# Kernel tuning notes

Hardware: AMD Instinct MI355X
Metric: run time of the kernel (lower is better)

Reference implementation:

```python
import jax, jax.numpy as jnp
import numpy as np

N, J, H, O, SD = 6144, 2000, 100, 6144, 2


def setup_inputs() -> dict:
    key = jax.random.key(0)
    ks = jax.random.split(key, 18)
    sc = lambda fan_in: 1.0 / np.sqrt(fan_in)
    inp = {
        "gene_expr": jax.random.normal(ks[0], (N, J), jnp.float32),
        "spatial_pos": jax.random.normal(ks[1], (N, SD), jnp.float32),
        # linear weights stored [in, out] (y = x @ W + b)
        "Wq": jax.random.normal(ks[2], (J, H), jnp.float32) * sc(J),
        "bq": jnp.zeros((H,), jnp.float32),
        "Wk": jax.random.normal(ks[3], (J, H), jnp.float32) * sc(J),
        "bk": jnp.zeros((H,), jnp.float32),
        "Wv": jax.random.normal(ks[4], (J, O), jnp.float32) * sc(J),
        "bv": jnp.zeros((O,), jnp.float32),
        "Ws": jax.random.normal(ks[5], (SD, H), jnp.float32) * sc(SD),
        "bs": jnp.zeros((H,), jnp.float32),
        "W1": jax.random.normal(ks[6], (H, H), jnp.float32) * sc(H),
        "b1": jnp.zeros((H,), jnp.float32),
        "W2": jax.random.normal(ks[7], (H, H), jnp.float32) * sc(H),
        "b2": jnp.zeros((H,), jnp.float32),
        "Wf": jax.random.normal(ks[8], (H, 1), jnp.float32) * sc(H),
        "bf": jnp.zeros((1,), jnp.float32),
    }
    return inp


def reference(gene_expr, spatial_pos, Wq, bq, Wk, bk, Wv, bv, Ws, bs,
              W1, b1, W2, b2, Wf, bf):
    dk = jnp.sqrt(jnp.asarray(H, gene_expr.dtype))

    Q = gene_expr @ Wq + bq            # [N,H]
    K = gene_expr @ Wk + bk            # [N,H]
    V = gene_expr @ Wv + bv            # [N,O]

    # advanced spatial scalar + pairwise tanh difference
    sp = spatial_pos @ Ws + bs                             # [N,H]
    enh = jax.nn.relu(jnp.tanh(sp @ W1 + b1) @ W2 + b2)    # [N,H]
    f = (enh @ Wf + bf)[:, 0]                              # [N]
    fdiff = jnp.tanh(f[:, None] - f[None, :])              # [N,N]

    # gaussian kernel of squared pairwise distances (cdist p=2, sigma=1)
    sq = jnp.sum(spatial_pos * spatial_pos, axis=1)
    d2 = jnp.maximum(sq[:, None] + sq[None, :] - 2.0 * (spatial_pos @ spatial_pos.T), 0.0)
    spatial_sim = jnp.exp(-d2 / 2.0)                       # [N,N]

    # row-wise cosine similarity of gene expression
    norm = jnp.linalg.norm(gene_expr, axis=1, keepdims=True)
    xn = gene_expr / jnp.maximum(norm, 1e-12)
    cos_sim = xn @ xn.T                                    # [N,N]

    logits = (Q @ K.T) / dk + spatial_sim + cos_sim + fdiff
    attn = jax.nn.softmax(logits, axis=-1)                 # stable softmax == max-subtract in src
    out = attn @ V                                         # [N,O]
    return attn, out
```

## Files before the change

### kernel.cpp

```cpp
#include <hip/hip_runtime.h>
#include <stdint.h>
#include <math.h>

#define NN 6144
#define JJ 2000
#define HH 100
#define KB 2176
#define XOFF 128
#define KQK 2048

typedef __bf16 bf16;
typedef __bf16 bf16x8 __attribute__((ext_vector_type(8)));
typedef float f32x4 __attribute__((ext_vector_type(4)));

__device__ __forceinline__ void load_lds16(const void* g, void* l) {
  __builtin_amdgcn_global_load_lds(
      (const __attribute__((address_space(1))) void*)(uintptr_t)g,
      (__attribute__((address_space(3))) void*)(uint32_t)(uintptr_t)l,
      16, 0, 0);
}

template <int MODE>
__global__ __launch_bounds__(256, 2) void gemm_bt(
    const bf16* __restrict__ A, const bf16* __restrict__ B,
    int lda, int ldb, int kdim,
    const float* __restrict__ p0, const float* __restrict__ p1,
    const float* __restrict__ p2,
    bf16* __restrict__ ob0, bf16* __restrict__ ob1,
    float* __restrict__ of0, float* __restrict__ rowsum)
{
  __shared__ alignas(16) bf16 As[128 * 64];
  __shared__ alignas(16) bf16 Bs[128 * 64];

  const int tid = threadIdx.x;
  const int lane = tid & 63;
  const int wv = tid >> 6;
  const int m0 = blockIdx.x * 128;
  const int n0 = blockIdx.y * 128;

  const int srow = lane >> 3;
  const int scol = ((lane & 7) ^ srow) * 8;
  const bf16* gA = A + (size_t)(m0 + wv * 32 + srow) * lda + scol;
  const bf16* gB = B + (size_t)(n0 + wv * 32 + srow) * ldb + scol;
  bf16* lA0 = &As[(wv * 32) * 64];
  bf16* lB0 = &Bs[(wv * 32) * 64];

  const int l15 = lane & 15;
  const int l4 = lane >> 4;
  const int s7 = l15 & 7;
  const int wm = (wv >> 1) * 64;
  const int wn = (wv & 1) * 64;
  const bf16* ra0 = &As[(wm + l15) * 64 + ((l4 ^ s7) * 8)];
  const bf16* ra1 = &As[(wm + l15) * 64 + (((l4 + 4) ^ s7) * 8)];
  const bf16* rb0 = &Bs[(wn + l15) * 64 + ((l4 ^ s7) * 8)];
  const bf16* rb1 = &Bs[(wn + l15) * 64 + (((l4 + 4) ^ s7) * 8)];

  f32x4 acc[4][4];
#pragma unroll
  for (int i = 0; i < 4; ++i)
#pragma unroll
    for (int j = 0; j < 4; ++j) acc[i][j] = {0.f, 0.f, 0.f, 0.f};

  const int kiters = kdim >> 6;
  for (int kt = 0; kt < kiters; ++kt) {
    __syncthreads();
#pragma unroll
    for (int it = 0; it < 4; ++it) {
      load_lds16(gA + (size_t)it * 8 * lda, lA0 + it * 512);
      load_lds16(gB + (size_t)it * 8 * ldb, lB0 + it * 512);
    }
    gA += 64;
    gB += 64;
    __syncthreads();
#pragma unroll
    for (int ks = 0; ks < 2; ++ks) {
      const bf16* ra = ks ? ra1 : ra0;
      const bf16* rb = ks ? rb1 : rb0;
      bf16x8 af[4], bb[4];
#pragma unroll
      for (int i = 0; i < 4; ++i)
        af[i] = *(const bf16x8*)(ra + i * 1024);
#pragma unroll
      for (int j = 0; j < 4; ++j)
        bb[j] = *(const bf16x8*)(rb + j * 1024);
#pragma unroll
      for (int i = 0; i < 4; ++i)
#pragma unroll
        for (int j = 0; j < 4; ++j)
          acc[i][j] = __builtin_amdgcn_mfma_f32_16x16x32_bf16(af[i], bb[j], acc[i][j], 0, 0, 0);
    }
  }

  const int row_base = m0 + wm + l4 * 4;
  const int col_base = n0 + wn + l15;

  if (MODE == 0) {
    float sqc[4], fc[4], pxc[4], pyc[4];
#pragma unroll
    for (int j = 0; j < 4; ++j) {
      int c = col_base + j * 16;
      sqc[j] = p0[c];
      fc[j] = p1[c];
      pxc[j] = p2[2 * c];
      pyc[j] = p2[2 * c + 1];
    }
#pragma unroll
    for (int i = 0; i < 4; ++i) {
#pragma unroll
      for (int r = 0; r < 4; ++r) {
        int row = row_base + i * 16 + r;
        float sqr = p0[row], fr = p1[row];
        float pxr = p2[2 * row], pyr = p2[2 * row + 1];
        float rs = 0.f;
#pragma unroll
        for (int j = 0; j < 4; ++j) {
          int c = col_base + j * 16;
          float d2 = fmaxf(sqr + sqc[j] - 2.f * (pxr * pxc[j] + pyr * pyc[j]), 0.f);
          float lg = acc[i][j][r] + __expf(-0.5f * d2) + tanhf(fr - fc[j]);
          float e = __expf(lg);
          ob0[(size_t)row * NN + c] = (bf16)e;
          rs += e;
        }
        rs += __shfl_xor(rs, 1);
        rs += __shfl_xor(rs, 2);
        rs += __shfl_xor(rs, 4);
        rs += __shfl_xor(rs, 8);
        if (l15 == 0) atomicAdd(&rowsum[row], rs);
      }
    }
  } else if (MODE == 1) {
    float nc[4];
#pragma unroll
    for (int j = 0; j < 4; ++j) nc[j] = p0[col_base + j * 16];
#pragma unroll
    for (int i = 0; i < 4; ++i) {
#pragma unroll
      for (int r = 0; r < 4; ++r) {
        int row = row_base + i * 16 + r;
        float bvr = p1[row];
#pragma unroll
        for (int j = 0; j < 4; ++j)
          ob0[(size_t)row * NN + col_base + j * 16] = (bf16)(acc[i][j][r] * nc[j] + bvr);
      }
    }
  } else if (MODE == 2) {
#pragma unroll
    for (int i = 0; i < 4; ++i) {
#pragma unroll
      for (int r = 0; r < 4; ++r) {
        int row = row_base + i * 16 + r;
        float rinv = 1.f / p0[row];
#pragma unroll
        for (int j = 0; j < 4; ++j)
          of0[(size_t)row * NN + col_base + j * 16] = acc[i][j][r] * rinv;
      }
    }
  } else {
#pragma unroll
    for (int i = 0; i < 4; ++i) {
#pragma unroll
      for (int r = 0; r < 4; ++r) {
        int row = row_base + i * 16 + r;
        float nm = p0[row];
#pragma unroll
        for (int j = 0; j < 4; ++j) {
          int h = col_base + j * 16;
          float v = acc[i][j][r] * nm;
          if (h < HH) ob0[(size_t)row * KB + h] = (bf16)((v + p1[h]) * 0.1f);
          else if (h < 2 * HH) ob1[(size_t)row * KB + (h - HH)] = (bf16)(v + p2[h - HH]);
        }
      }
    }
  }
}

__global__ void prep_xn(const float* __restrict__ gene, bf16* __restrict__ Ab,
                        bf16* __restrict__ Bb, float* __restrict__ normv)
{
  int row = blockIdx.x, tid = threadIdx.x;
  const float* g = gene + (size_t)row * JJ;
  float s = 0.f;
  for (int k = tid; k < JJ; k += 256) { float v = g[k]; s += v * v; }
#pragma unroll
  for (int m = 32; m >= 1; m >>= 1) s += __shfl_xor(s, m);
  __shared__ float red[4];
  if ((tid & 63) == 0) red[tid >> 6] = s;
  __syncthreads();
  float tot = red[0] + red[1] + red[2] + red[3];
  float nrm = sqrtf(tot);
  float rinv = 1.f / fmaxf(nrm, 1e-12f);
  if (tid == 0) normv[row] = nrm;
  bf16* a = Ab + (size_t)row * KB;
  bf16* b = Bb + (size_t)row * KB;
  for (int k = tid; k < JJ; k += 256) {
    bf16 v = (bf16)(g[k] * rinv);
    a[XOFF + k] = v;
    b[XOFF + k] = v;
  }
  if (tid < 28) { a[HH + tid] = (bf16)0.f; b[HH + tid] = (bf16)0.f; }
  if (tid < 48) { a[XOFF + JJ + tid] = (bf16)0.f; b[XOFF + JJ + tid] = (bf16)0.f; }
}

__global__ void prep_sf(const float* __restrict__ spos,
                        const float* __restrict__ Ws, const float* __restrict__ bs,
                        const float* __restrict__ W1, const float* __restrict__ b1,
                        const float* __restrict__ W2, const float* __restrict__ b2,
                        const float* __restrict__ Wf, const float* __restrict__ bfp,
                        float* __restrict__ sqv, float* __restrict__ fv)
{
  int row = blockIdx.x, tid = threadIdx.x;
  float px = spos[2 * row], py = spos[2 * row + 1];
  if (tid == 0) sqv[row] = px * px + py * py;
  __shared__ float sp[HH], t1[HH], e2[HH];
  if (tid < HH) sp[tid] = px * Ws[tid] + py * Ws[HH + tid] + bs[tid];
  __syncthreads();
  if (tid < HH) {
    float s = b1[tid];
    for (int gi = 0; gi < HH; ++gi) s += sp[gi] * W1[gi * HH + tid];
    t1[tid] = tanhf(s);
  }
  __syncthreads();
  if (tid < HH) {
    float s = b2[tid];
    for (int gi = 0; gi < HH; ++gi) s += t1[gi] * W2[gi * HH + tid];
    e2[tid] = fmaxf(s, 0.f) * Wf[tid];
  }
  __syncthreads();
  if (tid < 64) {
    float s = e2[tid] + ((tid < 36) ? e2[tid + 64] : 0.f);
#pragma unroll
    for (int m = 32; m >= 1; m >>= 1) s += __shfl_xor(s, m);
    if (tid == 0) fv[row] = s + bfp[0];
  }
}

__global__ void pack_wqk(const float* __restrict__ Wq, const float* __restrict__ Wk,
                         bf16* __restrict__ Wt)
{
  int idx = blockIdx.x * 256 + threadIdx.x;
  int h = idx >> 11;
  int k = idx & 2047;
  float v = 0.f;
  if (k < JJ) {
    if (h < HH) v = Wq[(size_t)k * HH + h];
    else if (h < 2 * HH) v = Wk[(size_t)k * HH + (h - HH)];
  }
  Wt[idx] = (bf16)v;
}

__global__ void pack_wvt(const float* __restrict__ Wv, bf16* __restrict__ Wt)
{
  __shared__ float tile[32][33];
  int tx = threadIdx.x & 31, ty = threadIdx.x >> 5;
  int o0 = blockIdx.x * 32, j0 = blockIdx.y * 32;
#pragma unroll
  for (int rr = 0; rr < 32; rr += 8) {
    int j = j0 + ty + rr;
    tile[ty + rr][tx] = (j < JJ) ? Wv[(size_t)j * NN + o0 + tx] : 0.f;
  }
  __syncthreads();
#pragma unroll
  for (int rr = 0; rr < 32; rr += 8) {
    int o = o0 + ty + rr;
    Wt[(size_t)o * KB + XOFF + j0 + tx] = (bf16)tile[tx][ty + rr];
  }
}

__global__ void zero_wvt_head(bf16* __restrict__ Wt)
{
  int idx = blockIdx.x * 256 + threadIdx.x;
  int o = idx >> 7, c = idx & 127;
  Wt[(size_t)o * KB + c] = (bf16)0.f;
}

__global__ void norm_attn(const bf16* __restrict__ P, const float* __restrict__ rowsum,
                          float* __restrict__ attn)
{
  int row = blockIdx.x;
  float rinv = 1.f / rowsum[row];
  const bf16x8* p = (const bf16x8*)(P + (size_t)row * NN);
  float* dst = attn + (size_t)row * NN;
  for (int c = threadIdx.x; c < NN / 8; c += 256) {
    bf16x8 v = p[c];
#pragma unroll
    for (int e = 0; e < 8; ++e) dst[c * 8 + e] = (float)v[e] * rinv;
  }
}

extern "C" void kernel_launch(void* const* d_in, const int* in_sizes, int n_in,
                              void* d_out, int out_size, void* d_ws, size_t ws_size,
                              hipStream_t stream)
{
  const float* gene = (const float*)d_in[0];
  const float* spos = (const float*)d_in[1];
  const float* Wq = (const float*)d_in[2];
  const float* bq = (const float*)d_in[3];
  const float* Wk = (const float*)d_in[4];
  const float* bk = (const float*)d_in[5];
  const float* Wv = (const float*)d_in[6];
  const float* bv = (const float*)d_in[7];
  const float* Ws = (const float*)d_in[8];
  const float* bs = (const float*)d_in[9];
  const float* W1 = (const float*)d_in[10];
  const float* b1 = (const float*)d_in[11];
  const float* W2 = (const float*)d_in[12];
  const float* b2 = (const float*)d_in[13];
  const float* Wf = (const float*)d_in[14];
  const float* bfp = (const float*)d_in[15];

  char* ws = (char*)d_ws;
  bf16* Abig = (bf16*)ws;            ws += (size_t)NN * KB * 2;
  bf16* Bbig = (bf16*)ws;            ws += (size_t)NN * KB * 2;
  bf16* WvT  = (bf16*)ws;            ws += (size_t)NN * KB * 2;
  bf16* WqkT = (bf16*)ws;            ws += (size_t)256 * KQK * 2;
  bf16* P    = (bf16*)ws;            ws += (size_t)NN * NN * 2;
  float* rowsum = (float*)ws;        ws += (size_t)NN * 4;
  float* normv  = (float*)ws;        ws += (size_t)NN * 4;
  float* sqv    = (float*)ws;        ws += (size_t)NN * 4;
  float* fv     = (float*)ws;        ws += (size_t)NN * 4;

  float* attn = (float*)d_out;
  float* outp = (float*)d_out + (size_t)NN * NN;
  bf16* Vt = (bf16*)d_out;

  hipMemsetAsync(rowsum, 0, NN * sizeof(float), stream);
  prep_xn<<<NN, 256, 0, stream>>>(gene, Abig, Bbig, normv);
  prep_sf<<<NN, 128, 0, stream>>>(spos, Ws, bs, W1, b1, W2, b2, Wf, bfp, sqv, fv);
  pack_wqk<<<(256 * KQK) / 256, 256, 0, stream>>>(Wq, Wk, WqkT);
  pack_wvt<<<dim3(NN / 32, KQK / 32), 256, 0, stream>>>(Wv, WvT);
  zero_wvt_head<<<(NN * XOFF) / 256, 256, 0, stream>>>(WvT);

  gemm_bt<3><<<dim3(NN / 128, 2), 256, 0, stream>>>(
      Abig + XOFF, WqkT, KB, KQK, KQK, normv, bq, bk, Abig, Bbig, nullptr, nullptr);
  gemm_bt<0><<<dim3(NN / 128, NN / 128), 256, 0, stream>>>(
      Abig, Bbig, KB, KB, KB, sqv, fv, spos, P, nullptr, nullptr, rowsum);
  gemm_bt<1><<<dim3(NN / 128, NN / 128), 256, 0, stream>>>(
      WvT, Bbig, KB, KB, KB, normv, bv, nullptr, Vt, nullptr, nullptr, nullptr);
  gemm_bt<2><<<dim3(NN / 128, NN / 128), 256, 0, stream>>>(
      P, Vt, NN, NN, NN, rowsum, nullptr, nullptr, nullptr, nullptr, outp, nullptr);
  norm_attn<<<NN, 256, 0, stream>>>(P, rowsum, attn);
}
```

Baseline: 1.291 ms.

## Replace 128-tile GEMMs with 256x256 pipelined kernel and merge logits/V GEMMs

Adds a 256x256-tile, 512-thread GEMM core with swizzled LDS, double-buffered direct-to-LDS loads, interleaved MFMA phases with setprio, and a block-index swizzle for L2 locality. The logits and V GEMMs, which share the B operand, now run as a single launch split over blockIdx.z, and P@V uses the same core. The aim is more data reuse per tile and fewer launches, traded against much higher register and LDS pressure and more complex barrier and waitcnt choreography.

```diff
diff --git a/kernel.cpp b/kernel.cpp
--- a/kernel.cpp
+++ b/kernel.cpp
@@ -95,22 +95,221 @@
   const int col_base = n0 + wn + l15;
 
   if (MODE == 0) {
+  } else if (MODE == 1) {
+  } else if (MODE == 2) {
+  } else {
+#pragma unroll
+    for (int i = 0; i < 4; ++i) {
+#pragma unroll
+      for (int r = 0; r < 4; ++r) {
+        int row = row_base + i * 16 + r;
+        float nm = p0[row];
+#pragma unroll
+        for (int j = 0; j < 4; ++j) {
+          int h = col_base + j * 16;
+          float v = acc[i][j][r] * nm;
+          if (h < HH) ob0[(size_t)row * KB + h] = (bf16)((v + p1[h]) * 0.1f);
+          else if (h < 2 * HH) ob1[(size_t)row * KB + (h - HH)] = (bf16)(v + p2[h - HH]);
+        }
+      }
+    }
+  }
+}
+
+__device__ __forceinline__ void gemm256_core(
+    const bf16* __restrict__ A, const bf16* __restrict__ B,
+    int lda, int ldb, int kdim, int m0, int n0, f32x4 (&acc)[8][4])
+{
+  __shared__ alignas(16) bf16 As[2][256 * 64];
+  __shared__ alignas(16) bf16 Bs[2][256 * 64];
+
+  const int tid = threadIdx.x;
+  const int lane = tid & 63;
+  const int wv = tid >> 6;
+  const int wm = wv >> 2;
+  const int wn = wv & 3;
+  const int l15 = lane & 15;
+  const int l4 = lane >> 4;
+  const int s7 = lane & 7;
+  const int srow = lane >> 3;
+  const int scol = ((lane & 7) ^ srow) * 8;
+
+  const bf16* gA = A + (size_t)(m0 + wv * 8 + srow) * lda + scol;
+  const bf16* gB = B + (size_t)(n0 + wv * 8 + srow) * ldb + scol;
+
+  const int c0 = (l4 ^ s7) * 8;
+  const int c1 = ((l4 + 4) ^ s7) * 8;
+
+#pragma unroll
+  for (int i = 0; i < 8; ++i)
+#pragma unroll
+    for (int j = 0; j < 4; ++j) acc[i][j] = {0.f, 0.f, 0.f, 0.f};
+
+  const int kt = kdim >> 6;
+
+#define SA_(bufi, h, T)                                                        \
+  do {                                                                         \
+    load_lds16(gA + (size_t)((h) * 128) * lda + (size_t)(T) * 64,              \
+               &As[(bufi)][(wv * 8 + (h) * 128) * 64]);                        \
+    load_lds16(gA + (size_t)((h) * 128 + 64) * lda + (size_t)(T) * 64,         \
+               &As[(bufi)][(wv * 8 + (h) * 128 + 64) * 64]);                   \
+  } while (0)
+#define SB_(bufi, h, T)                                                        \
+  do {                                                                         \
+    load_lds16(gB + (size_t)((h) * 128) * ldb + (size_t)(T) * 64,              \
+               &Bs[(bufi)][(wv * 8 + (h) * 128) * 64]);                        \
+    load_lds16(gB + (size_t)((h) * 128 + 64) * ldb + (size_t)(T) * 64,         \
+               &Bs[(bufi)][(wv * 8 + (h) * 128 + 64) * 64]);                   \
+  } while (0)
+
+  SB_(0, 0, 0); SA_(0, 0, 0); SB_(0, 1, 0); SA_(0, 1, 0);
+  SB_(1, 0, 1); SA_(1, 0, 1); SA_(1, 1, 1);
+  asm volatile("s_waitcnt vmcnt(6)" ::: "memory");
+  __builtin_amdgcn_s_barrier();
+
+  bf16x8 af[4][2], b0[2][2], b1[2][2];
+
+  for (int t2 = 0; t2 < kt; t2 += 2) {
+#pragma unroll
+    for (int u = 0; u < 2; ++u) {
+      const int T = t2 + u;
+      const int buf = u, bufn = u ^ 1;
+      const bf16* pA = &As[buf][(wm * 128 + l15) * 64];
+      const bf16* pB = &Bs[buf][(wn * 64 + l15) * 64];
+
+#pragma unroll
+      for (int fm = 0; fm < 4; ++fm) {
+        af[fm][0] = *(const bf16x8*)(pA + (fm * 16) * 64 + c0);
+        af[fm][1] = *(const bf16x8*)(pA + (fm * 16) * 64 + c1);
+      }
+#pragma unroll
+      for (int fn = 0; fn < 2; ++fn) {
+        b0[fn][0] = *(const bf16x8*)(pB + (fn * 16) * 64 + c0);
+        b0[fn][1] = *(const bf16x8*)(pB + (fn * 16) * 64 + c1);
+      }
+      if (T + 1 < kt) SB_(bufn, 1, T + 1);
+      __builtin_amdgcn_s_barrier();
+      asm volatile("s_waitcnt lgkmcnt(0)" ::: "memory");
+      __builtin_amdgcn_sched_barrier(0);
+      __builtin_amdgcn_s_setprio(1);
+#pragma unroll
+      for (int ks = 0; ks < 2; ++ks)
+#pragma unroll
+        for (int fm = 0; fm < 4; ++fm)
+#pragma unroll
+          for (int fn = 0; fn < 2; ++fn)
+            acc[fm][fn] = __builtin_amdgcn_mfma_f32_16x16x32_bf16(
+                af[fm][ks], b0[fn][ks], acc[fm][fn], 0, 0, 0);
+      __builtin_amdgcn_s_setprio(0);
+      __builtin_amdgcn_s_barrier();
+
+#pragma unroll
+      for (int fn = 0; fn < 2; ++fn) {
+        b1[fn][0] = *(const bf16x8*)(pB + ((32 + fn * 16) * 64) + c0);
+        b1[fn][1] = *(const bf16x8*)(pB + ((32 + fn * 16) * 64) + c1);
+      }
+      __builtin_amdgcn_s_barrier();
+      asm volatile("s_waitcnt lgkmcnt(0)" ::: "memory");
+      __builtin_amdgcn_sched_barrier(0);
+      __builtin_amdgcn_s_setprio(1);
+#pragma unroll
+      for (int ks = 0; ks < 2; ++ks)
+#pragma unroll
+        for (int fm = 0; fm < 4; ++fm)
+#pragma unroll
+          for (int fn = 0; fn < 2; ++fn)
+            acc[fm][2 + fn] = __builtin_amdgcn_mfma_f32_16x16x32_bf16(
+                af[fm][ks], b1[fn][ks], acc[fm][2 + fn], 0, 0, 0);
+      __builtin_amdgcn_s_setprio(0);
+      __builtin_amdgcn_s_barrier();
+
+#pragma unroll
+      for (int fm = 0; fm < 4; ++fm) {
+        af[fm][0] = *(const bf16x8*)(pA + ((64 + fm * 16) * 64) + c0);
+        af[fm][1] = *(const bf16x8*)(pA + ((64 + fm * 16) * 64) + c1);
+      }
+      if (T + 2 < kt) SB_(buf, 0, T + 2);
+      __builtin_amdgcn_s_barrier();
+      asm volatile("s_waitcnt lgkmcnt(0)" ::: "memory");
+      __builtin_amdgcn_sched_barrier(0);
+      __builtin_amdgcn_s_setprio(1);
+#pragma unroll
+      for (int ks = 0; ks < 2; ++ks)
+#pragma unroll
+        for (int fm = 0; fm < 4; ++fm)
+#pragma unroll
+          for (int fn = 0; fn < 2; ++fn)
+            acc[4 + fm][2 + fn] = __builtin_amdgcn_mfma_f32_16x16x32_bf16(
+                af[fm][ks], b1[fn][ks], acc[4 + fm][2 + fn], 0, 0, 0);
+      __builtin_amdgcn_s_setprio(0);
+      __builtin_amdgcn_s_barrier();
+
+      if (T + 2 < kt) { SA_(buf, 0, T + 2); SA_(buf, 1, T + 2); }
+      __builtin_amdgcn_s_barrier();
+      __builtin_amdgcn_s_setprio(1);
+#pragma unroll
+      for (int ks = 0; ks < 2; ++ks)
+#pragma unroll
+        for (int fm = 0; fm < 4; ++fm)
+#pragma unroll
+          for (int fn = 0; fn < 2; ++fn)
+            acc[4 + fm][fn] = __builtin_amdgcn_mfma_f32_16x16x32_bf16(
+                af[fm][ks], b0[fn][ks], acc[4 + fm][fn], 0, 0, 0);
+      __builtin_amdgcn_s_setprio(0);
+      if (T + 1 < kt) {
+        if (T + 2 < kt) asm volatile("s_waitcnt vmcnt(6)" ::: "memory");
+        else            asm volatile("s_waitcnt vmcnt(0)" ::: "memory");
+      }
+      __builtin_amdgcn_s_barrier();
+    }
+  }
+#undef SA_
+#undef SB_
+}
+
+__global__ __launch_bounds__(512, 2) void gemm256_lv(
+    const bf16* __restrict__ Abig, const bf16* __restrict__ WvT,
+    const bf16* __restrict__ Bbig,
+    const float* __restrict__ sqv, const float* __restrict__ fv,
+    const float* __restrict__ spos, const float* __restrict__ normv,
+    const float* __restrict__ bv,
+    bf16* __restrict__ P, bf16* __restrict__ Vt, float* __restrict__ rowsum)
+{
+  const int GB = NN / 256;
+  int lin = blockIdx.y * GB + blockIdx.x;
+  int swz = (lin & 7) * ((GB * GB) / 8) + (lin >> 3);
+  const int m0 = (swz % GB) * 256;
+  const int n0 = (swz / GB) * 256;
+  const bool isl = (blockIdx.z == 0);
+
+  f32x4 acc[8][4];
+  gemm256_core(isl ? Abig : WvT, Bbig, KB, KB, KB, m0, n0, acc);
+
+  const int tid = threadIdx.x;
+  const int lane = tid & 63;
+  const int wv = tid >> 6;
+  const int wm = wv >> 2, wn = wv & 3;
+  const int l15 = lane & 15, l4 = lane >> 4;
+  const int row_base = m0 + wm * 128 + l4 * 4;
+  const int col_base = n0 + wn * 64 + l15;
+
+  if (isl) {
     float sqc[4], fc[4], pxc[4], pyc[4];
 #pragma unroll
     for (int j = 0; j < 4; ++j) {
       int c = col_base + j * 16;
-      sqc[j] = p0[c];
-      fc[j] = p1[c];
-      pxc[j] = p2[2 * c];
-      pyc[j] = p2[2 * c + 1];
-    }
-#pragma unroll
-    for (int i = 0; i < 4; ++i) {
+      sqc[j] = sqv[c];
+      fc[j] = fv[c];
+      pxc[j] = spos[2 * c];
+      pyc[j] = spos[2 * c + 1];
+    }
+#pragma unroll
+    for (int i = 0; i < 8; ++i) {
 #pragma unroll
       for (int r = 0; r < 4; ++r) {
         int row = row_base + i * 16 + r;
-        float sqr = p0[row], fr = p1[row];
-        float pxr = p2[2 * row], pyr = p2[2 * row + 1];
+        float sqr = sqv[row], fr = fv[row];
+        float pxr = spos[2 * row], pyr = spos[2 * row + 1];
         float rs = 0.f;
 #pragma unroll
         for (int j = 0; j < 4; ++j) {
@@ -118,7 +317,7 @@
           float d2 = fmaxf(sqr + sqc[j] - 2.f * (pxr * pxc[j] + pyr * pyc[j]), 0.f);
           float lg = acc[i][j][r] + __expf(-0.5f * d2) + tanhf(fr - fc[j]);
           float e = __expf(lg);
-          ob0[(size_t)row * NN + c] = (bf16)e;
+          P[(size_t)row * NN + c] = (bf16)e;
           rs += e;
         }
         rs += __shfl_xor(rs, 1);
@@ -128,48 +327,53 @@
         if (l15 == 0) atomicAdd(&rowsum[row], rs);
       }
     }
-  } else if (MODE == 1) {
+  } else {
     float nc[4];
 #pragma unroll
-    for (int j = 0; j < 4; ++j) nc[j] = p0[col_base + j * 16];
-#pragma unroll
-    for (int i = 0; i < 4; ++i) {
+    for (int j = 0; j < 4; ++j) nc[j] = normv[col_base + j * 16];
+#pragma unroll
+    for (int i = 0; i < 8; ++i) {
 #pragma unroll
       for (int r = 0; r < 4; ++r) {
         int row = row_base + i * 16 + r;
-        float bvr = p1[row];
+        float bvr = bv[row];
 #pragma unroll
         for (int j = 0; j < 4; ++j)
-          ob0[(size_t)row * NN + col_base + j * 16] = (bf16)(acc[i][j][r] * nc[j] + bvr);
-      }
-    }
-  } else if (MODE == 2) {
-#pragma unroll
-    for (int i = 0; i < 4; ++i) {
-#pragma unroll
-      for (int r = 0; r < 4; ++r) {
-        int row = row_base + i * 16 + r;
-        float rinv = 1.f / p0[row];
-#pragma unroll
-        for (int j = 0; j < 4; ++j)
-          of0[(size_t)row * NN + col_base + j * 16] = acc[i][j][r] * rinv;
-      }
-    }
-  } else {
-#pragma unroll
-    for (int i = 0; i < 4; ++i) {
-#pragma unroll
-      for (int r = 0; r < 4; ++r) {
-        int row = row_base + i * 16 + r;
-        float nm = p0[row];
-#pragma unroll
-        for (int j = 0; j < 4; ++j) {
-          int h = col_base + j * 16;
-          float v = acc[i][j][r] * nm;
-          if (h < HH) ob0[(size_t)row * KB + h] = (bf16)((v + p1[h]) * 0.1f);
-          else if (h < 2 * HH) ob1[(size_t)row * KB + (h - HH)] = (bf16)(v + p2[h - HH]);
-        }
-      }
+          Vt[(size_t)row * NN + col_base + j * 16] = (bf16)(acc[i][j][r] * nc[j] + bvr);
+      }
+    }
+  }
+}
+
+__global__ __launch_bounds__(512, 2) void gemm256_pv(
+    const bf16* __restrict__ Pm, const bf16* __restrict__ Vt,
+    const float* __restrict__ rowsum, float* __restrict__ outp)
+{
+  const int GB = NN / 256;
+  int lin = blockIdx.y * GB + blockIdx.x;
+  int swz = (lin & 7) * ((GB * GB) / 8) + (lin >> 3);
+  const int m0 = (swz % GB) * 256;
+  const int n0 = (swz / GB) * 256;
+
+  f32x4 acc[8][4];
+  gemm256_core(Pm, Vt, NN, NN, NN, m0, n0, acc);
+
+  const int tid = threadIdx.x;
+  const int lane = tid & 63;
+  const int wv = tid >> 6;
+  const int wm = wv >> 2, wn = wv & 3;
+  const int l15 = lane & 15, l4 = lane >> 4;
+  const int row_base = m0 + wm * 128 + l4 * 4;
+  const int col_base = n0 + wn * 64 + l15;
+#pragma unroll
+  for (int i = 0; i < 8; ++i) {
+#pragma unroll
+    for (int r = 0; r < 4; ++r) {
+      int row = row_base + i * 16 + r;
+      float rinv = 1.f / rowsum[row];
+#pragma unroll
+      for (int j = 0; j < 4; ++j)
+        outp[(size_t)row * NN + col_base + j * 16] = acc[i][j][r] * rinv;
     }
   }
 }
@@ -332,11 +536,8 @@
 
   gemm_bt<3><<<dim3(NN / 128, 2), 256, 0, stream>>>(
       Abig + XOFF, WqkT, KB, KQK, KQK, normv, bq, bk, Abig, Bbig, nullptr, nullptr);
-  gemm_bt<0><<<dim3(NN / 128, NN / 128), 256, 0, stream>>>(
-      Abig, Bbig, KB, KB, KB, sqv, fv, spos, P, nullptr, nullptr, rowsum);
-  gemm_bt<1><<<dim3(NN / 128, NN / 128), 256, 0, stream>>>(
-      WvT, Bbig, KB, KB, KB, normv, bv, nullptr, Vt, nullptr, nullptr, nullptr);
-  gemm_bt<2><<<dim3(NN / 128, NN / 128), 256, 0, stream>>>(
-      P, Vt, NN, NN, NN, rowsum, nullptr, nullptr, nullptr, nullptr, outp, nullptr);
+  gemm256_lv<<<dim3(NN / 256, NN / 256, 2), 512, 0, stream>>>(
+      Abig, WvT, Bbig, sqv, fv, spos, normv, bv, P, Vt, rowsum);
+  gemm256_pv<<<dim3(NN / 256, NN / 256), 512, 0, stream>>>(P, Vt, rowsum, outp);
   norm_attn<<<NN, 256, 0, stream>>>(P, rowsum, attn);
 }
```

Result: no change. 1.315 ms (+1.9%).
